# Optimization experiments

Hardware: AMD Instinct MI355X
Metric: run time of the kernel (lower is better)

## Reference

```python
import jax, jax.numpy as jnp
import numpy as np

N_NODES = 100000


def gcn_conv(x, edge_index, W, b, n_nodes):
    # PyG GCNConv: add self-loops, symmetric normalization, linear, scatter-add, bias.
    src, dst = edge_index[0], edge_index[1]
    loop = jnp.arange(n_nodes, dtype=edge_index.dtype)
    src = jnp.concatenate([src, loop])  # [E + N]
    dst = jnp.concatenate([dst, loop])
    # degree of target nodes (edge weight = 1)
    deg = jax.ops.segment_sum(jnp.ones_like(dst, dtype=x.dtype), dst,
                              num_segments=n_nodes)
    dinv = jnp.where(deg > 0, jax.lax.rsqrt(deg), 0.0)
    norm = dinv[src] * dinv[dst]  # [E + N]
    h = x @ W  # [N, out] small dense GEMM
    msg = h[src] * norm[:, None]  # gather + scale (memory-bound)
    out = jax.ops.segment_sum(msg, dst, num_segments=n_nodes)
    return out + b


def setup_inputs() -> dict:
    key = jax.random.key(0)
    k = jax.random.split(key, 6)
    n, e = N_NODES, 1600000
    d_in, d_hid, d_out = 128, 128, 64
    x = jax.random.normal(k[0], (n, d_in), dtype=jnp.float32)
    edge_index = jax.random.randint(k[1], (2, e), 0, n, dtype=jnp.int64)
    W1 = jax.random.normal(k[2], (d_in, d_hid), dtype=jnp.float32) / np.sqrt(d_in)
    b1 = jnp.zeros((d_hid,), dtype=jnp.float32)
    W2 = jax.random.normal(k[3], (d_hid, d_out), dtype=jnp.float32) / np.sqrt(d_hid)
    b2 = jnp.zeros((d_out,), dtype=jnp.float32)
    return {"x": x, "edge_index": edge_index, "W1": W1, "b1": b1,
            "W2": W2, "b2": b2}


def reference(x, edge_index, W1, b1, W2, b2):
    n = x.shape[0]
    h = gcn_conv(x, edge_index, W1, b1, n)
    h = jax.nn.relu(h)
    return gcn_conv(h, edge_index, W2, b2, n)
```

## Files before the change

### kernel.cpp

```cpp
#include <hip/hip_runtime.h>

typedef __attribute__((ext_vector_type(8))) short bf16x8;
typedef __attribute__((ext_vector_type(4))) float f32x4;

#define NBINS 391
#define NBLK  196
#define ECHUNK 8192


__device__ __forceinline__ unsigned short f2bf(float f) {
    unsigned u = __float_as_uint(f);
    u += 0x7fffu + ((u >> 16) & 1u);
    return (unsigned short)(u >> 16);
}
__device__ __forceinline__ float bf_lo(unsigned u) { return __uint_as_float(u << 16); }
__device__ __forceinline__ float bf_hi(unsigned u) { return __uint_as_float(u & 0xffff0000u); }


__global__ __launch_bounds__(256) void bucket_hist(const int* __restrict__ ei, int E, int n,
                                                   int* __restrict__ hist_t) {
    __shared__ int h[NBINS];
    int t = threadIdx.x, blk = blockIdx.x;
    for (int i = t; i < NBINS; i += 256) h[i] = 0;
    __syncthreads();
    int start = blk * ECHUNK;
    int end = min(E, start + ECHUNK);
    for (int i = start + t; i < end; i += 256) {
        int s = ei[i];
        int d = ei[E + i];
        if ((unsigned)d < (unsigned)n && (unsigned)s < (unsigned)n)
            atomicAdd(&h[d >> 8], 1);
    }
    __syncthreads();
    for (int i = t; i < NBINS; i += 256) hist_t[i * NBLK + blk] = h[i];
}

__global__ __launch_bounds__(256) void scan_partial(const int* __restrict__ in,
                                                    int ntot, int* __restrict__ blocksum) {
    int base = blockIdx.x * 1024;
    int t = threadIdx.x;
    int s = 0;
#pragma unroll
    for (int j = 0; j < 4; ++j) {
        int i = base + (t << 2) + j;
        if (i < ntot) s += in[i];
    }
#pragma unroll
    for (int off = 1; off < 64; off <<= 1) s += __shfl_xor(s, off);
    __shared__ int ws[4];
    if ((t & 63) == 0) ws[t >> 6] = s;
    __syncthreads();
    if (t == 0) blocksum[blockIdx.x] = ws[0] + ws[1] + ws[2] + ws[3];
}

__global__ __launch_bounds__(256) void scan_blocksums(int* __restrict__ blocksum, int nb) {
    __shared__ int sh[256];
    int t = threadIdx.x;
    sh[t] = (t < nb) ? blocksum[t] : 0;
    __syncthreads();
#pragma unroll
    for (int off = 1; off < 256; off <<= 1) {
        int v = (t >= off) ? sh[t - off] : 0;
        __syncthreads();
        sh[t] += v;
        __syncthreads();
    }
    if (t < nb) blocksum[t] = (t == 0) ? 0 : sh[t - 1];
}

__global__ __launch_bounds__(256) void scan2_final(const int* __restrict__ in,
                                                   const int* __restrict__ blockoff,
                                                   int ntot, int* __restrict__ out) {
    int base = blockIdx.x * 1024;
    int t = threadIdx.x;
    int v[4];
    int s = 0;
#pragma unroll
    for (int j = 0; j < 4; ++j) {
        int i = base + (t << 2) + j;
        v[j] = (i < ntot) ? in[i] : 0;
        s += v[j];
    }
    __shared__ int sh[256];
    sh[t] = s;
    __syncthreads();
#pragma unroll
    for (int off = 1; off < 256; off <<= 1) {
        int x = (t >= off) ? sh[t - off] : 0;
        __syncthreads();
        sh[t] += x;
        __syncthreads();
    }
    int run = blockoff[blockIdx.x] + (sh[t] - s);
#pragma unroll
    for (int j = 0; j < 4; ++j) {
        int i = base + (t << 2) + j;
        if (i < ntot) {
            out[i] = run;
            run += v[j];
        }
    }
    int lo = base + (t << 2);
    if (lo <= ntot - 1 && ntot - 1 < lo + 4) out[ntot] = run;
}

__global__ __launch_bounds__(256) void bucket_scatter(const int* __restrict__ ei, int E, int n,
                                                      const int* __restrict__ off,
                                                      unsigned long long* __restrict__ ebuf) {
    __shared__ int lo[NBINS];
    int t = threadIdx.x, blk = blockIdx.x;
    for (int i = t; i < NBINS; i += 256) lo[i] = off[i * NBLK + blk];
    __syncthreads();
    int start = blk * ECHUNK;
    int end = min(E, start + ECHUNK);
    for (int i = start + t; i < end; i += 256) {
        int s = ei[i];
        int d = ei[E + i];
        if ((unsigned)d < (unsigned)n && (unsigned)s < (unsigned)n) {
            int pos = atomicAdd(&lo[d >> 8], 1);
            if (pos < E) ebuf[pos] = ((unsigned long long)(unsigned)d << 32) | (unsigned)s;
        }
    }
}

__global__ __launch_bounds__(256) void bucket_csr(const unsigned long long* __restrict__ ebuf,
                                                  const int* __restrict__ off, int E, int n,
                                                  int* __restrict__ rowptr,
                                                  float* __restrict__ dinv,
                                                  int* __restrict__ srcs) {
    int b = blockIdx.x;
    int t = threadIdx.x;
    int bstart = off[b * NBLK];
    int bend = off[(b + 1) * NBLK];
    __shared__ int cnt[256], sh[256], basev[256], fill[256];
    cnt[t] = 0;
    __syncthreads();
    for (int i = bstart + t; i < bend; i += 256) {
        int d = (int)(ebuf[i] >> 32);
        atomicAdd(&cnt[d & 255], 1);
    }
    __syncthreads();
    int myc = cnt[t];
    sh[t] = myc;
    __syncthreads();
#pragma unroll
    for (int o = 1; o < 256; o <<= 1) {
        int v = (t >= o) ? sh[t - o] : 0;
        __syncthreads();
        sh[t] += v;
        __syncthreads();
    }
    int incl = sh[t];
    int base = bstart + incl - myc;
    basev[t] = base;
    fill[t] = 0;
    int d = b * 256 + t;
    if (d < n) {
        rowptr[d] = base;
        dinv[d] = rsqrtf((float)(myc + 1));
        if (d == n - 1) rowptr[n] = bstart + incl;
    }
    __syncthreads();
    for (int i = bstart + t; i < bend; i += 256) {
        unsigned long long p = ebuf[i];
        int dl = (int)(p >> 32) & 255;
        int s = (int)(p & 0xffffffffu);
        int r = atomicAdd(&fill[dl], 1);
        srcs[basev[dl] + r] = s;
    }
}


__global__ __launch_bounds__(256) void prep_w(const float* __restrict__ W1,
                                              const float* __restrict__ W2,
                                              unsigned short* __restrict__ Wt1,
                                              unsigned short* __restrict__ Wt2) {
    int t = blockIdx.x * blockDim.x + threadIdx.x;
    if (t < 128 * 128) {
        int k = t >> 7, c = t & 127;
        Wt1[c * 128 + k] = f2bf(W1[t]);
    } else if (t < 128 * 128 + 128 * 64) {
        int i = t - 128 * 128;
        int k = i >> 6, c = i & 63;
        Wt2[c * 128 + k] = f2bf(W2[i]);
    }
}


template <int M, bool IN_BF16>
__global__ __launch_bounds__(256) void gemm_mfma(const void* __restrict__ Xv,
                                                 const unsigned short* __restrict__ Wt,
                                                 const float* __restrict__ dinv,
                                                 unsigned short* __restrict__ G16,
                                                 int n, int ntiles) {
    constexpr int K = 128;
    constexpr int BM = 64;
    __shared__ unsigned short Xs[BM * K];
    __shared__ unsigned short Wl[M * K];
    int t = threadIdx.x;

#pragma unroll
    for (int i = 0; i < M / 16; ++i) {
        int f = t + i * 256;
        int c = f >> 4, k8 = f & 15;
        uint4 v = ((const uint4*)Wt)[f];
        int addr = (c * 256 + k8 * 16) ^ ((c & 7) << 4);
        *(uint4*)((char*)Wl + addr) = v;
    }

    int w = t >> 6, l = t & 63;
    int lg = l >> 4, lm = l & 15;
    constexpr int NCT = M / 16;
    union F8 { uint2 u2[2]; bf16x8 v; };

    for (int tile = blockIdx.x; tile < ntiles; tile += gridDim.x) {
        int blockRow = tile * BM;
        __syncthreads();

        if (!IN_BF16) {
            const float* X = (const float*)Xv;
#pragma unroll
            for (int i = 0; i < 8; ++i) {
                int f = t + i * 256;
                int m = f >> 5, k4 = f & 31;
                float4 v = make_float4(0.f, 0.f, 0.f, 0.f);
                if (blockRow + m < n) v = ((const float4*)(X + (size_t)(blockRow + m) * K))[k4];
                uint2 p;
                p.x = (unsigned)f2bf(v.x) | ((unsigned)f2bf(v.y) << 16);
                p.y = (unsigned)f2bf(v.z) | ((unsigned)f2bf(v.w) << 16);
                int addr = (m * 256 + k4 * 8) ^ ((m & 7) << 4);
                *(uint2*)((char*)Xs + addr) = p;
            }
        } else {
            const unsigned short* X = (const unsigned short*)Xv;
#pragma unroll
            for (int i = 0; i < 4; ++i) {
                int f = t + i * 256;
                int m = f >> 4, k8 = f & 15;
                uint4 v = make_uint4(0u, 0u, 0u, 0u);
                if (blockRow + m < n) v = ((const uint4*)(X + (size_t)(blockRow + m) * K))[k8];
                int addr = (m * 256 + k8 * 16) ^ ((m & 7) << 4);
                *(uint4*)((char*)Xs + addr) = v;
            }
        }
        __syncthreads();

        bf16x8 afr[4];
        int mrow = 16 * w + lm;
        int swa = (mrow & 7) << 4;
#pragma unroll
        for (int kk = 0; kk < 4; ++kk) {
            int pa = mrow * 256 + (32 * kk + 4 * lg) * 2;
            F8 a;
            a.u2[0] = *(const uint2*)((const char*)Xs + (pa ^ swa));
            a.u2[1] = *(const uint2*)((const char*)Xs + ((pa + 32) ^ swa));
            afr[kk] = a.v;
        }

        f32x4 acc[NCT];
#pragma unroll
        for (int ct = 0; ct < NCT; ++ct) acc[ct] = (f32x4){0.f, 0.f, 0.f, 0.f};

#pragma unroll
        for (int ct = 0; ct < NCT; ++ct) {
            int c = ct * 16 + lm;
            int swc = (c & 7) << 4;
#pragma unroll
            for (int kk = 0; kk < 4; ++kk) {
                int pb = c * 256 + (32 * kk + 4 * lg) * 2;
                F8 b;
                b.u2[0] = *(const uint2*)((const char*)Wl + (pb ^ swc));
                b.u2[1] = *(const uint2*)((const char*)Wl + ((pb + 32) ^ swc));
                acc[ct] = __builtin_amdgcn_mfma_f32_16x16x32_bf16(afr[kk], b.v, acc[ct], 0, 0, 0);
            }
        }

        float dv[4];
#pragma unroll
        for (int q = 0; q < 4; ++q) {
            int r = blockRow + 16 * w + 4 * lg + q;
            dv[q] = (r < n) ? dinv[r] : 0.f;
        }
#pragma unroll
        for (int ct = 0; ct < NCT; ++ct) {
#pragma unroll
            for (int q = 0; q < 4; ++q) {
                int r = blockRow + 16 * w + 4 * lg + q;
                if (r < n) G16[(size_t)r * M + ct * 16 + lm] = f2bf(acc[ct][q] * dv[q]);
            }
        }
    }
}


__global__ __launch_bounds__(256) void agg_d128(const unsigned short* __restrict__ G16,
                                                const int* __restrict__ srcs,
                                                const int* __restrict__ rowptr,
                                                const float* __restrict__ dinv,
                                                const float* __restrict__ bias,
                                                unsigned short* __restrict__ out, int n) {
    int wid = (blockIdx.x * blockDim.x + threadIdx.x) >> 6;
    int lane = threadIdx.x & 63;
    if (wid >= n) return;
    int g = lane >> 4;
    int lh = lane & 15;

    float acc[8];
    {
        uint4 u = make_uint4(0u, 0u, 0u, 0u);
        if (g == 0) u = ((const uint4*)(G16 + (size_t)wid * 128))[lh];
        acc[0] = bf_lo(u.x); acc[1] = bf_hi(u.x);
        acc[2] = bf_lo(u.y); acc[3] = bf_hi(u.y);
        acc[4] = bf_lo(u.z); acc[5] = bf_hi(u.z);
        acc[6] = bf_lo(u.w); acc[7] = bf_hi(u.w);
    }

    int beg = rowptr[wid], end = rowptr[wid + 1];
    for (int base = beg; base < end; base += 64) {
        int m = end - base;
        if (m > 64) m = 64;
        int sv = (base + lane < end) ? srcs[base + lane] : 0;
        for (int j = 0; j < m; j += 4) {
            int s = __shfl(sv, j + g);
            uint4 u = ((const uint4*)(G16 + (size_t)s * 128))[lh];
            if (j + g >= m) u = make_uint4(0u, 0u, 0u, 0u);
            acc[0] += bf_lo(u.x); acc[1] += bf_hi(u.x);
            acc[2] += bf_lo(u.y); acc[3] += bf_hi(u.y);
            acc[4] += bf_lo(u.z); acc[5] += bf_hi(u.z);
            acc[6] += bf_lo(u.w); acc[7] += bf_hi(u.w);
        }
    }

#pragma unroll
    for (int k = 0; k < 8; ++k) {
        acc[k] += __shfl_xor(acc[k], 16);
        acc[k] += __shfl_xor(acc[k], 32);
    }

    if (g < 2) {
        float di = dinv[wid];
        int idx = 2 * lh + g;
        float4 b = ((const float4*)bias)[idx];
        int k0 = 4 * g;
        float o0 = fmaxf(acc[k0 + 0] * di + b.x, 0.f);
        float o1 = fmaxf(acc[k0 + 1] * di + b.y, 0.f);
        float o2 = fmaxf(acc[k0 + 2] * di + b.z, 0.f);
        float o3 = fmaxf(acc[k0 + 3] * di + b.w, 0.f);
        uint2 p;
        p.x = (unsigned)f2bf(o0) | ((unsigned)f2bf(o1) << 16);
        p.y = (unsigned)f2bf(o2) | ((unsigned)f2bf(o3) << 16);
        ((uint2*)(out + (size_t)wid * 128))[idx] = p;
    }
}

__global__ __launch_bounds__(256) void agg_d64(const unsigned short* __restrict__ G16,
                                               const int* __restrict__ srcs,
                                               const int* __restrict__ rowptr,
                                               const float* __restrict__ dinv,
                                               const float* __restrict__ bias,
                                               float* __restrict__ out, int n) {
    int wid = (blockIdx.x * blockDim.x + threadIdx.x) >> 6;
    int lane = threadIdx.x & 63;
    if (wid >= n) return;
    int g = lane >> 3;
    int lh = lane & 7;

    float acc[8];
    {
        uint4 u = make_uint4(0u, 0u, 0u, 0u);
        if (g == 0) u = ((const uint4*)(G16 + (size_t)wid * 64))[lh];
        acc[0] = bf_lo(u.x); acc[1] = bf_hi(u.x);
        acc[2] = bf_lo(u.y); acc[3] = bf_hi(u.y);
        acc[4] = bf_lo(u.z); acc[5] = bf_hi(u.z);
        acc[6] = bf_lo(u.w); acc[7] = bf_hi(u.w);
    }

    int beg = rowptr[wid], end = rowptr[wid + 1];
    for (int base = beg; base < end; base += 64) {
        int m = end - base;
        if (m > 64) m = 64;
        int sv = (base + lane < end) ? srcs[base + lane] : 0;
        for (int j = 0; j < m; j += 8) {
            int s = __shfl(sv, j + g);
            uint4 u = ((const uint4*)(G16 + (size_t)s * 64))[lh];
            if (j + g >= m) u = make_uint4(0u, 0u, 0u, 0u);
            acc[0] += bf_lo(u.x); acc[1] += bf_hi(u.x);
            acc[2] += bf_lo(u.y); acc[3] += bf_hi(u.y);
            acc[4] += bf_lo(u.z); acc[5] += bf_hi(u.z);
            acc[6] += bf_lo(u.w); acc[7] += bf_hi(u.w);
        }
    }

#pragma unroll
    for (int k = 0; k < 8; ++k) {
        acc[k] += __shfl_xor(acc[k], 8);
        acc[k] += __shfl_xor(acc[k], 16);
        acc[k] += __shfl_xor(acc[k], 32);
    }

    if (g < 2) {
        float di = dinv[wid];
        int idx = 2 * lh + g;
        float4 b = ((const float4*)bias)[idx];
        int k0 = 4 * g;
        float4 o;
        o.x = acc[k0 + 0] * di + b.x;
        o.y = acc[k0 + 1] * di + b.y;
        o.z = acc[k0 + 2] * di + b.z;
        o.w = acc[k0 + 3] * di + b.w;
        ((float4*)(out + (size_t)wid * 64))[idx] = o;
    }
}


extern "C" void kernel_launch(void* const* d_in, const int* in_sizes, int n_in,
                              void* d_out, int out_size, void* d_ws, size_t ws_size,
                              hipStream_t stream) {
    const float* x = (const float*)d_in[0];
    const int* ei = (const int*)d_in[1];
    const float* W1 = (const float*)d_in[2];
    const float* b1 = (const float*)d_in[3];
    const float* W2 = (const float*)d_in[4];
    const float* b2 = (const float*)d_in[5];
    float* out = (float*)d_out;

    const int n = in_sizes[0] / 128;
    const int E = in_sizes[1] / 2;
    const int ntot = NBINS * NBLK;

    char* ws = (char*)d_ws;
    size_t off_b = 0;
    auto alloc = [&](size_t bytes) {
        void* p = ws + off_b;
        off_b = (off_b + bytes + 255) & ~(size_t)255;
        return p;
    };
    unsigned short* g1 = (unsigned short*)alloc((size_t)n * 128 * 2);
    unsigned short* a1 = (unsigned short*)alloc((size_t)n * 128 * 2);
    int* rowptr = (int*)alloc(((size_t)n + 1) * 4);
    float* dinv = (float*)alloc((size_t)n * 4);
    int* srcs = (int*)alloc((size_t)E * 4);
    unsigned long long* ebuf = (unsigned long long*)alloc((size_t)E * 8);
    int* hist_t = (int*)alloc((size_t)ntot * 4);
    int* off = (int*)alloc(((size_t)ntot + 1) * 4);
    int* blocksum = (int*)alloc(1024 * 4);
    unsigned short* Wt1 = (unsigned short*)alloc(128 * 128 * 2);
    unsigned short* Wt2 = (unsigned short*)alloc(64 * 128 * 2);
    unsigned short* g2 = g1;

    const int nb_scan = (ntot + 1023) / 1024;
    const int ntiles = (n + 63) / 64;
    const int gb = 768;

    prep_w<<<96, 256, 0, stream>>>(W1, W2, Wt1, Wt2);
    bucket_hist<<<NBLK, 256, 0, stream>>>(ei, E, n, hist_t);
    scan_partial<<<nb_scan, 256, 0, stream>>>(hist_t, ntot, blocksum);
    scan_blocksums<<<1, 256, 0, stream>>>(blocksum, nb_scan);
    scan2_final<<<nb_scan, 256, 0, stream>>>(hist_t, blocksum, ntot, off);
    bucket_scatter<<<NBLK, 256, 0, stream>>>(ei, E, n, off, ebuf);
    bucket_csr<<<NBINS, 256, 0, stream>>>(ebuf, off, E, n, rowptr, dinv, srcs);

    gemm_mfma<128, false><<<gb, 256, 0, stream>>>(x, Wt1, dinv, g1, n, ntiles);
    agg_d128<<<(n + 3) / 4, 256, 0, stream>>>(g1, srcs, rowptr, dinv, b1, a1, n);

    gemm_mfma<64, true><<<gb, 256, 0, stream>>>(a1, Wt2, dinv, g2, n, ntiles);
    agg_d64<<<(n + 3) / 4, 256, 0, stream>>>(g2, srcs, rowptr, dinv, b2, out, n);
}
```

Measured before the change: 221.2 us.

## Pad CSR rows to multiples of four with zero sentinel row, unroll gathers

CSR neighbor lists are padded to multiples of 4 using a sentinel source index n that points at an added all-zero row in G. This removes the per-iteration bounds masking in the aggregation loops. The inner gather loop is unrolled to issue two independent row loads per step. agg_d64 is remapped to 16 lanes of uint2 per row, and agg_d128 stores its output as full uint4 from one group. The cost is extra padding entries to gather and a larger srcs buffer.

```diff
diff --git a/kernel.cpp b/kernel.cpp
--- a/kernel.cpp
+++ b/kernel.cpp
@@ -6,6 +6,7 @@
 #define NBINS 391
 #define NBLK  196
 #define ECHUNK 8192
+#define BKTPAD 1024
 
 
 __device__ __forceinline__ unsigned short f2bf(float f) {
@@ -15,6 +16,17 @@
 }
 __device__ __forceinline__ float bf_lo(unsigned u) { return __uint_as_float(u << 16); }
 __device__ __forceinline__ float bf_hi(unsigned u) { return __uint_as_float(u & 0xffff0000u); }
+
+__device__ __forceinline__ void acc8(float* a, uint4 u) {
+    a[0] += bf_lo(u.x); a[1] += bf_hi(u.x);
+    a[2] += bf_lo(u.y); a[3] += bf_hi(u.y);
+    a[4] += bf_lo(u.z); a[5] += bf_hi(u.z);
+    a[6] += bf_lo(u.w); a[7] += bf_hi(u.w);
+}
+__device__ __forceinline__ void acc4(float* a, uint2 u) {
+    a[0] += bf_lo(u.x); a[1] += bf_hi(u.x);
+    a[2] += bf_lo(u.y); a[3] += bf_hi(u.y);
+}
 
 
 __global__ __launch_bounds__(256) void bucket_hist(const int* __restrict__ ei, int E, int n,
@@ -126,12 +138,14 @@
 __global__ __launch_bounds__(256) void bucket_csr(const unsigned long long* __restrict__ ebuf,
                                                   const int* __restrict__ off, int E, int n,
                                                   int* __restrict__ rowptr,
+                                                  int* __restrict__ rend,
                                                   float* __restrict__ dinv,
                                                   int* __restrict__ srcs) {
     int b = blockIdx.x;
     int t = threadIdx.x;
     int bstart = off[b * NBLK];
     int bend = off[(b + 1) * NBLK];
+    int pstart = bstart + b * BKTPAD;
     __shared__ int cnt[256], sh[256], basev[256], fill[256];
     cnt[t] = 0;
     __syncthreads();
@@ -141,7 +155,8 @@
     }
     __syncthreads();
     int myc = cnt[t];
-    sh[t] = myc;
+    int pmyc = (myc + 3) & ~3;
+    sh[t] = pmyc;
     __syncthreads();
 #pragma unroll
     for (int o = 1; o < 256; o <<= 1) {
@@ -150,15 +165,16 @@
         sh[t] += v;
         __syncthreads();
     }
-    int incl = sh[t];
-    int base = bstart + incl - myc;
-    basev[t] = base;
+    int pincl = sh[t];
+    int pbase = pstart + pincl - pmyc;
+    basev[t] = pbase;
     fill[t] = 0;
     int d = b * 256 + t;
     if (d < n) {
-        rowptr[d] = base;
+        rowptr[d] = pbase;
+        rend[d] = pbase + pmyc;
         dinv[d] = rsqrtf((float)(myc + 1));
-        if (d == n - 1) rowptr[n] = bstart + incl;
+        for (int r = myc; r < pmyc; ++r) srcs[pbase + r] = n;
     }
     __syncthreads();
     for (int i = bstart + t; i < bend; i += 256) {
@@ -174,7 +190,9 @@
 __global__ __launch_bounds__(256) void prep_w(const float* __restrict__ W1,
                                               const float* __restrict__ W2,
                                               unsigned short* __restrict__ Wt1,
-                                              unsigned short* __restrict__ Wt2) {
+                                              unsigned short* __restrict__ Wt2,
+                                              unsigned short* __restrict__ g1,
+                                              unsigned short* __restrict__ g2, int n) {
     int t = blockIdx.x * blockDim.x + threadIdx.x;
     if (t < 128 * 128) {
         int k = t >> 7, c = t & 127;
@@ -183,6 +201,10 @@
         int i = t - 128 * 128;
         int k = i >> 6, c = i & 63;
         Wt2[c * 128 + k] = f2bf(W2[i]);
+    } else if (t < 128 * 128 + 128 * 64 + 128) {
+        g1[(size_t)n * 128 + (t - 128 * 128 - 128 * 64)] = 0;
+    } else if (t < 128 * 128 + 128 * 64 + 192) {
+        g2[(size_t)n * 64 + (t - 128 * 128 - 128 * 64 - 128)] = 0;
     }
 }
 
@@ -296,6 +318,7 @@
 __global__ __launch_bounds__(256) void agg_d128(const unsigned short* __restrict__ G16,
                                                 const int* __restrict__ srcs,
                                                 const int* __restrict__ rowptr,
+                                                const int* __restrict__ rend,
                                                 const float* __restrict__ dinv,
                                                 const float* __restrict__ bias,
                                                 unsigned short* __restrict__ out, int n) {
@@ -308,26 +331,31 @@
     float acc[8];
     {
         uint4 u = make_uint4(0u, 0u, 0u, 0u);
-        if (g == 0) u = ((const uint4*)(G16 + (size_t)wid * 128))[lh];
+        if (g == 0) u = ((const uint4*)G16)[(size_t)wid * 16 + lh];
         acc[0] = bf_lo(u.x); acc[1] = bf_hi(u.x);
         acc[2] = bf_lo(u.y); acc[3] = bf_hi(u.y);
         acc[4] = bf_lo(u.z); acc[5] = bf_hi(u.z);
         acc[6] = bf_lo(u.w); acc[7] = bf_hi(u.w);
     }
 
-    int beg = rowptr[wid], end = rowptr[wid + 1];
+    int beg = rowptr[wid], end = rend[wid];
     for (int base = beg; base < end; base += 64) {
-        int m = end - base;
-        if (m > 64) m = 64;
-        int sv = (base + lane < end) ? srcs[base + lane] : 0;
-        for (int j = 0; j < m; j += 4) {
-            int s = __shfl(sv, j + g);
-            uint4 u = ((const uint4*)(G16 + (size_t)s * 128))[lh];
-            if (j + g >= m) u = make_uint4(0u, 0u, 0u, 0u);
-            acc[0] += bf_lo(u.x); acc[1] += bf_hi(u.x);
-            acc[2] += bf_lo(u.y); acc[3] += bf_hi(u.y);
-            acc[4] += bf_lo(u.z); acc[5] += bf_hi(u.z);
-            acc[6] += bf_lo(u.w); acc[7] += bf_hi(u.w);
+        int mm = end - base;
+        if (mm > 64) mm = 64;
+        int sv = (base + lane < end) ? srcs[base + lane] : n;
+        int j = 0;
+        for (; j + 8 <= mm; j += 8) {
+            int s0 = __shfl(sv, j + g);
+            int s1 = __shfl(sv, j + 4 + g);
+            uint4 u0 = ((const uint4*)G16)[(size_t)s0 * 16 + lh];
+            uint4 u1 = ((const uint4*)G16)[(size_t)s1 * 16 + lh];
+            acc8(acc, u0);
+            acc8(acc, u1);
+        }
+        if (j < mm) {
+            int s0 = __shfl(sv, j + g);
+            uint4 u0 = ((const uint4*)G16)[(size_t)s0 * 16 + lh];
+            acc8(acc, u0);
         }
     }
 
@@ -337,78 +365,85 @@
         acc[k] += __shfl_xor(acc[k], 32);
     }
 
-    if (g < 2) {
+    if (g == 0) {
         float di = dinv[wid];
-        int idx = 2 * lh + g;
-        float4 b = ((const float4*)bias)[idx];
-        int k0 = 4 * g;
-        float o0 = fmaxf(acc[k0 + 0] * di + b.x, 0.f);
-        float o1 = fmaxf(acc[k0 + 1] * di + b.y, 0.f);
-        float o2 = fmaxf(acc[k0 + 2] * di + b.z, 0.f);
-        float o3 = fmaxf(acc[k0 + 3] * di + b.w, 0.f);
-        uint2 p;
-        p.x = (unsigned)f2bf(o0) | ((unsigned)f2bf(o1) << 16);
-        p.y = (unsigned)f2bf(o2) | ((unsigned)f2bf(o3) << 16);
-        ((uint2*)(out + (size_t)wid * 128))[idx] = p;
+        float4 b0 = ((const float4*)bias)[2 * lh];
+        float4 b1 = ((const float4*)bias)[2 * lh + 1];
+        float o[8];
+        o[0] = fmaxf(acc[0] * di + b0.x, 0.f);
+        o[1] = fmaxf(acc[1] * di + b0.y, 0.f);
+        o[2] = fmaxf(acc[2] * di + b0.z, 0.f);
+        o[3] = fmaxf(acc[3] * di + b0.w, 0.f);
+        o[4] = fmaxf(acc[4] * di + b1.x, 0.f);
+        o[5] = fmaxf(acc[5] * di + b1.y, 0.f);
+        o[6] = fmaxf(acc[6] * di + b1.z, 0.f);
+        o[7] = fmaxf(acc[7] * di + b1.w, 0.f);
+        uint4 p;
+        p.x = (unsigned)f2bf(o[0]) | ((unsigned)f2bf(o[1]) << 16);
+        p.y = (unsigned)f2bf(o[2]) | ((unsigned)f2bf(o[3]) << 16);
+        p.z = (unsigned)f2bf(o[4]) | ((unsigned)f2bf(o[5]) << 16);
+        p.w = (unsigned)f2bf(o[6]) | ((unsigned)f2bf(o[7]) << 16);
+        ((uint4*)(out + (size_t)wid * 128))[lh] = p;
     }
 }
 
 __global__ __launch_bounds__(256) void agg_d64(const unsigned short* __restrict__ G16,
                                                const int* __restrict__ srcs,
                                                const int* __restrict__ rowptr,
+                                               const int* __restrict__ rend,
                                                const float* __restrict__ dinv,
                                                const float* __restrict__ bias,
                                                float* __restrict__ out, int n) {
     int wid = (blockIdx.x * blockDim.x + threadIdx.x) >> 6;
     int lane = threadIdx.x & 63;
     if (wid >= n) return;
-    int g = lane >> 3;
-    int lh = lane & 7;
-
-    float acc[8];
+    int g = lane >> 4;
+    int lh = lane & 15;
+
+    float acc[4];
     {
-        uint4 u = make_uint4(0u, 0u, 0u, 0u);
-        if (g == 0) u = ((const uint4*)(G16 + (size_t)wid * 64))[lh];
+        uint2 u = make_uint2(0u, 0u);
+        if (g == 0) u = ((const uint2*)G16)[(size_t)wid * 16 + lh];
         acc[0] = bf_lo(u.x); acc[1] = bf_hi(u.x);
         acc[2] = bf_lo(u.y); acc[3] = bf_hi(u.y);
-        acc[4] = bf_lo(u.z); acc[5] = bf_hi(u.z);
-        acc[6] = bf_lo(u.w); acc[7] = bf_hi(u.w);
-    }
-
-    int beg = rowptr[wid], end = rowptr[wid + 1];
+    }
+
+    int beg = rowptr[wid], end = rend[wid];
     for (int base = beg; base < end; base += 64) {
-        int m = end - base;
-        if (m > 64) m = 64;
-        int sv = (base + lane < end) ? srcs[base + lane] : 0;
-        for (int j = 0; j < m; j += 8) {
-            int s = __shfl(sv, j + g);
-            uint4 u = ((const uint4*)(G16 + (size_t)s * 64))[lh];
-            if (j + g >= m) u = make_uint4(0u, 0u, 0u, 0u);
-            acc[0] += bf_lo(u.x); acc[1] += bf_hi(u.x);
-            acc[2] += bf_lo(u.y); acc[3] += bf_hi(u.y);
-            acc[4] += bf_lo(u.z); acc[5] += bf_hi(u.z);
-            acc[6] += bf_lo(u.w); acc[7] += bf_hi(u.w);
-        }
-    }
-
-#pragma unroll
-    for (int k = 0; k < 8; ++k) {
-        acc[k] += __shfl_xor(acc[k], 8);
+        int mm = end - base;
+        if (mm > 64) mm = 64;
+        int sv = (base + lane < end) ? srcs[base + lane] : n;
+        int j = 0;
+        for (; j + 8 <= mm; j += 8) {
+            int s0 = __shfl(sv, j + g);
+            int s1 = __shfl(sv, j + 4 + g);
+            uint2 u0 = ((const uint2*)G16)[(size_t)s0 * 16 + lh];
+            uint2 u1 = ((const uint2*)G16)[(size_t)s1 * 16 + lh];
+            acc4(acc, u0);
+            acc4(acc, u1);
+        }
+        if (j < mm) {
+            int s0 = __shfl(sv, j + g);
+            uint2 u0 = ((const uint2*)G16)[(size_t)s0 * 16 + lh];
+            acc4(acc, u0);
+        }
+    }
+
+#pragma unroll
+    for (int k = 0; k < 4; ++k) {
         acc[k] += __shfl_xor(acc[k], 16);
         acc[k] += __shfl_xor(acc[k], 32);
     }
 
-    if (g < 2) {
+    if (g == 0) {
         float di = dinv[wid];
-        int idx = 2 * lh + g;
-        float4 b = ((const float4*)bias)[idx];
-        int k0 = 4 * g;
+        float4 b = ((const float4*)bias)[lh];
         float4 o;
-        o.x = acc[k0 + 0] * di + b.x;
-        o.y = acc[k0 + 1] * di + b.y;
-        o.z = acc[k0 + 2] * di + b.z;
-        o.w = acc[k0 + 3] * di + b.w;
-        ((float4*)(out + (size_t)wid * 64))[idx] = o;
+        o.x = acc[0] * di + b.x;
+        o.y = acc[1] * di + b.y;
+        o.z = acc[2] * di + b.z;
+        o.w = acc[3] * di + b.w;
+        ((float4*)(out + (size_t)wid * 64))[lh] = o;
     }
 }
 
@@ -435,34 +470,35 @@
         off_b = (off_b + bytes + 255) & ~(size_t)255;
         return p;
     };
-    unsigned short* g1 = (unsigned short*)alloc((size_t)n * 128 * 2);
+    unsigned short* g1 = (unsigned short*)alloc(((size_t)n + 1) * 128 * 2);
+    unsigned short* g2 = (unsigned short*)alloc(((size_t)n + 1) * 64 * 2);
     unsigned short* a1 = (unsigned short*)alloc((size_t)n * 128 * 2);
-    int* rowptr = (int*)alloc(((size_t)n + 1) * 4);
+    int* rowptr = (int*)alloc((size_t)n * 4);
+    int* rend = (int*)alloc((size_t)n * 4);
     float* dinv = (float*)alloc((size_t)n * 4);
-    int* srcs = (int*)alloc((size_t)E * 4);
+    int* srcs = (int*)alloc(((size_t)E + (size_t)NBINS * BKTPAD) * 4);
     unsigned long long* ebuf = (unsigned long long*)alloc((size_t)E * 8);
     int* hist_t = (int*)alloc((size_t)ntot * 4);
     int* off = (int*)alloc(((size_t)ntot + 1) * 4);
     int* blocksum = (int*)alloc(1024 * 4);
     unsigned short* Wt1 = (unsigned short*)alloc(128 * 128 * 2);
     unsigned short* Wt2 = (unsigned short*)alloc(64 * 128 * 2);
-    unsigned short* g2 = g1;
 
     const int nb_scan = (ntot + 1023) / 1024;
     const int ntiles = (n + 63) / 64;
     const int gb = 768;
 
-    prep_w<<<96, 256, 0, stream>>>(W1, W2, Wt1, Wt2);
+    prep_w<<<97, 256, 0, stream>>>(W1, W2, Wt1, Wt2, g1, g2, n);
     bucket_hist<<<NBLK, 256, 0, stream>>>(ei, E, n, hist_t);
     scan_partial<<<nb_scan, 256, 0, stream>>>(hist_t, ntot, blocksum);
     scan_blocksums<<<1, 256, 0, stream>>>(blocksum, nb_scan);
     scan2_final<<<nb_scan, 256, 0, stream>>>(hist_t, blocksum, ntot, off);
     bucket_scatter<<<NBLK, 256, 0, stream>>>(ei, E, n, off, ebuf);
-    bucket_csr<<<NBINS, 256, 0, stream>>>(ebuf, off, E, n, rowptr, dinv, srcs);
+    bucket_csr<<<NBINS, 256, 0, stream>>>(ebuf, off, E, n, rowptr, rend, dinv, srcs);
 
     gemm_mfma<128, false><<<gb, 256, 0, stream>>>(x, Wt1, dinv, g1, n, ntiles);
-    agg_d128<<<(n + 3) / 4, 256, 0, stream>>>(g1, srcs, rowptr, dinv, b1, a1, n);
+    agg_d128<<<(n + 3) / 4, 256, 0, stream>>>(g1, srcs, rowptr, rend, dinv, b1, a1, n);
 
     gemm_mfma<64, true><<<gb, 256, 0, stream>>>(a1, Wt2, dinv, g2, n, ntiles);
-    agg_d64<<<(n + 3) / 4, 256, 0, stream>>>(g2, srcs, rowptr, dinv, b2, out, n);
-}
+    agg_d64<<<(n + 3) / 4, 256, 0, stream>>>(g2, srcs, rowptr, rend, dinv, b2, out, n);
+}
```

Result: faster. 213.3 us (-3.6%).
